# Performance work log

Hardware: AMD Instinct MI355X
Metric: run time of the kernel (lower is better)

Reference implementation:

```python
import jax, jax.numpy as jnp
import numpy as np

ALPHA = 0.2
N_NODES = 50000
N_REL = 500
E = 500000
E_NHOP = 100000


def l2norm(v):
    n = jnp.sqrt(jnp.sum(v * v, axis=1, keepdims=True))
    return v / jnp.maximum(n, 1e-12)


def sp_attention(x, src, dst, edge_embed, a, a2, concat):
    # a: [out, 2*din + drel]; edge_m = a @ cat(x[src], x[dst], edge_embed).T, done blockwise
    N, din = x.shape
    a_src, a_dst, a_rel = a[:, :din], a[:, din:2 * din], a[:, 2 * din:]
    edge_m = x[src] @ a_src.T + x[dst] @ a_dst.T + edge_embed @ a_rel.T  # [E, out]
    powers = -jax.nn.leaky_relu(edge_m @ a2, ALPHA)                      # [E]
    edge_e = jnp.exp(powers)
    e_rowsum = jax.ops.segment_sum(edge_e, src, num_segments=N)
    e_rowsum = jnp.where(e_rowsum == 0.0, 1e-12, e_rowsum)
    h_prime = jax.ops.segment_sum(edge_e[:, None] * edge_m, src, num_segments=N)
    h_prime = h_prime / e_rowsum[:, None]
    return jax.nn.elu(h_prime) if concat else h_prime


def spgat(x, rel, src, dst, edge_type, et_nhop, head_params, W, out_a, out_a2):
    ee = jnp.concatenate([rel[edge_type], rel[et_nhop[:, 0]] + rel[et_nhop[:, 1]]], axis=0)
    x = jnp.concatenate([sp_attention(x, src, dst, ee, a, a2, True) for a, a2 in head_params], axis=1)
    out_rel = rel @ W
    ee2 = jnp.concatenate([out_rel[edge_type], out_rel[et_nhop[:, 0]] + out_rel[et_nhop[:, 1]]], axis=0)
    x = jax.nn.elu(sp_attention(x, src, dst, ee2, out_a, out_a2, False))
    return x, out_rel


def forward_impl(entity_emb, relation_emb, W_entities,
                 g0_a0, g0_s0, g0_a1, g0_s1, g0_W, g0_oa, g0_os,
                 g1_a0, g1_s0, g1_W, g1_oa, g1_os,
                 edge_list, edge_type, train_indices_nhop, batch_inputs):
    ent = l2norm(entity_emb)
    rel = l2norm(relation_emb)
    # n-hop edges: (col3 -> col0), relation pair in cols 1,2
    src = jnp.concatenate([edge_list[0], train_indices_nhop[:, 3]])
    dst = jnp.concatenate([edge_list[1], train_indices_nhop[:, 0]])
    et_nhop = train_indices_nhop[:, 1:3]
    mask = jnp.zeros((ent.shape[0],), ent.dtype).at[batch_inputs[:, 2]].set(1.0)
    # layer 0 (2 heads)
    ent_up = ent @ W_entities
    rel_up = rel @ W_entities
    e_new, r_new = spgat(ent, rel, src, dst, edge_type, et_nhop,
                         [(g0_a0, g0_s0), (g0_a1, g0_s1)], g0_W, g0_oa, g0_os)
    ent = l2norm(ent_up + mask[:, None] * e_new)
    rel = l2norm(rel_up + r_new)
    # layer 1 (1 head, residual)
    e_new, r_new = spgat(ent, rel, src, dst, edge_type, et_nhop,
                         [(g1_a0, g1_s0)], g1_W, g1_oa, g1_os)
    ent = l2norm(ent + mask[:, None] * e_new)
    rel = l2norm(rel + r_new)
    return ent, rel


def setup_inputs() -> dict:
    key = jax.random.key(0)
    ks = jax.random.split(key, 20)
    s = 0.05
    inp = {
        "entity_emb": jax.random.normal(ks[0], (N_NODES, 100), jnp.float32),
        "relation_emb": jax.random.normal(ks[1], (N_REL, 100), jnp.float32),
        "W_entities": jax.random.normal(ks[2], (100, 200), jnp.float32) * s,
        "g0_a0": jax.random.normal(ks[3], (100, 300), jnp.float32) * s,
        "g0_s0": jax.random.normal(ks[4], (100,), jnp.float32) * s,
        "g0_a1": jax.random.normal(ks[5], (100, 300), jnp.float32) * s,
        "g0_s1": jax.random.normal(ks[6], (100,), jnp.float32) * s,
        "g0_W": jax.random.normal(ks[7], (100, 200), jnp.float32) * s,
        "g0_oa": jax.random.normal(ks[8], (200, 600), jnp.float32) * s,
        "g0_os": jax.random.normal(ks[9], (200,), jnp.float32) * s,
        "g1_a0": jax.random.normal(ks[10], (200, 600), jnp.float32) * s,
        "g1_s0": jax.random.normal(ks[11], (200,), jnp.float32) * s,
        "g1_W": jax.random.normal(ks[12], (200, 200), jnp.float32) * s,
        "g1_oa": jax.random.normal(ks[13], (200, 600), jnp.float32) * s,
        "g1_os": jax.random.normal(ks[14], (200,), jnp.float32) * s,
        "edge_list": jax.random.randint(ks[15], (2, E), 0, N_NODES, jnp.int64 if jax.config.jax_enable_x64 else jnp.int32),
        "edge_type": jax.random.randint(ks[16], (E,), 0, N_REL),
        "train_indices_nhop": jax.random.randint(ks[17], (E_NHOP, 4), 0, N_REL),
        "batch_inputs": jax.random.randint(ks[18], (10000, 3), 0, N_NODES),
    }
    return inp


def reference(entity_emb, relation_emb, W_entities,
              g0_a0, g0_s0, g0_a1, g0_s1, g0_W, g0_oa, g0_os,
              g1_a0, g1_s0, g1_W, g1_oa, g1_os,
              edge_list, edge_type, train_indices_nhop, batch_inputs):
    return forward_impl(entity_emb, relation_emb, W_entities,
                        g0_a0, g0_s0, g0_a1, g0_s1, g0_W, g0_oa, g0_os,
                        g1_a0, g1_s0, g1_W, g1_oa, g1_os,
                        edge_list, edge_type, train_indices_nhop, batch_inputs)
```

## Files before the change

### kernel.cpp

```cpp
#include <hip/hip_runtime.h>
#include <hip/hip_bf16.h>
#include <cstdint>
#include <cstddef>

#define NNODES 50000
#define NRELS  500
#define NEDGE  500000
#define NETOT  600000
#define MP     50048
#define RPAD   512
#define HOTN   512

typedef __attribute__((ext_vector_type(8))) short bf16x8;
typedef __attribute__((ext_vector_type(4))) float f32x4;

__device__ inline float bf2f(unsigned short s){
  union { unsigned u; float f; } v; v.u = ((unsigned)s) << 16; return v.f;
}
__device__ inline unsigned short f2bf(float f){
  __hip_bfloat16 h = __float2bfloat16(f);
  return __builtin_bit_cast(unsigned short, h);
}
__device__ inline float rl_f(float v, int i){
  return __builtin_bit_cast(float, __builtin_amdgcn_readlane(__builtin_bit_cast(int, v), i));
}

struct WEnt { int src, ld, boff, rows, K, tr, dstoff, Kp, rp; };
__device__ const WEnt g_went[18] = {
  {0,200,0,200,100,1,      0,128,256},
  {3,200,0,200,100,1,  32768,128,256},
  {1,300,  0,100,100,0,  65536,128,128},
  {1,300,100,100,100,0,  81920,128,128},
  {2,300,  0,100,100,0,  98304,128,128},
  {2,300,100,100,100,0, 114688,128,128},
  {1,300,200,100,100,0, 131072,128,128},
  {2,300,200,100,100,0, 147456,128,128},
  {4,600,  0,200,200,0, 163840,224,256},
  {4,600,200,200,200,0, 221184,224,256},
  {4,600,400,200,200,0, 278528,224,256},
  {5,600,  0,200,200,0, 335872,224,256},
  {5,600,200,200,200,0, 393216,224,256},
  {5,600,400,200,200,0, 450560,224,256},
  {6,200,0,200,200,1,   507904,224,256},
  {7,600,  0,200,200,0, 565248,224,256},
  {7,600,200,200,200,0, 622592,224,256},
  {7,600,400,200,200,0, 679936,224,256},
};
struct Ptr8 { const float* p[8]; };

#define SB_O1 587
#define SB_O2 599
#define SB_O3 620
#define SB_O4 641
#define SB_O5 650
#define SB_O6 5342
#define SB_O7 5351
#define SB_O8 13415
#define SB_O9 25915
#define SB_TOT 26040

struct SetupArgs {
  int* iall;
  __hip_bfloat16 *aent0, *ax1, *aent1, *arel0, *arel1;
  float* wt;
  const float *s0h, *s1h, *os0, *s1l, *os1;
  __hip_bfloat16* wa;
  Ptr8 wsrcs;
  const float *entity, *relation;
};

__global__ __launch_bounds__(256) void k_setup(SetupArgs a){
  int bid = blockIdx.x, tid = threadIdx.x;
  if (bid < SB_O1){ int i = bid*256 + tid; if (i < 150001) a.iall[i] = 0; return; }
  if (bid < SB_O2){ int i = (bid-SB_O1)*256 + tid;
    ((int*)(a.aent0 + (size_t)NNODES*128))[i] = 0; return; }
  if (bid < SB_O3){ int i = (bid-SB_O2)*256 + tid;
    if (i < 5376) ((int*)(a.ax1 + (size_t)NNODES*224))[i] = 0; return; }
  if (bid < SB_O4){ int i = (bid-SB_O3)*256 + tid;
    if (i < 5376) ((int*)(a.aent1 + (size_t)NNODES*224))[i] = 0; return; }
  if (bid < SB_O5){ int i = (bid-SB_O4)*256 + tid;
    if (i < 768) ((int*)(a.arel0 + (size_t)NRELS*128))[i] = 0;
    else if (i < 2112) ((int*)(a.arel1 + (size_t)NRELS*224))[i - 768] = 0;
    return; }
  if (bid < SB_O6){ int i = (bid-SB_O5)*256 + tid;
    int r = i / 24, k = 200 + (i - r*24);
    a.ax1[(size_t)r*224 + k] = __float2bfloat16(0.f); return; }
  if (bid < SB_O7){
    int i = (bid-SB_O6)*256 + tid; if (i >= 2304) return;
    float v = 0.f;
    if (i < 512){ int c = i & 127; const float* s = (i < 256) ? a.s0h : a.s1h; if (c < 100) v = s[c]; }
    else if (i < 768){ int j2 = i - 512, c = j2 & 127; const float* s = (j2 < 128) ? a.s0h : a.s1h; if (c < 100) v = s[c]; }
    else { int j2 = i - 768, t = j2 >> 9, c = j2 & 255;
           const float* s = (t==0)?a.os0:(t==1)?a.s1l:a.os1; if (c < 200) v = s[c]; }
    a.wt[i] = v; return; }
  if (bid < SB_O8){
    int sb = bid - SB_O7;
    WEnt e = g_went[sb / 448];
    int i = (sb - (sb/448)*448)*256 + tid;
    if (i >= e.rp*e.Kp) return;
    int r = i / e.Kp, k = i - r*e.Kp;
    float v = 0.f;
    if (r < e.rows && k < e.K)
      v = e.tr ? a.wsrcs.p[e.src][(size_t)k*e.ld + r] : a.wsrcs.p[e.src][(size_t)r*e.ld + e.boff + k];
    a.wa[e.dstoff + i] = __float2bfloat16(v); return; }
  {
    int wave = tid >> 6, lane = tid & 63;
    const float* src; __hip_bfloat16* dst; int row;
// ... 75 lines not shown
  bool isE = n < NNODES;
  int row = isE ? n : n - NNODES;
  const __hip_bfloat16* b = (isE ? baseE : baseR) + (size_t)row*224;
  const __hip_bfloat16* h = (isE ? hE : hR) + (size_t)row*224;
  float m = isE ? mask[row] : 1.0f;
  int c = lane*4;
  float4 v = make_float4(0.f,0.f,0.f,0.f);
  if (c < 200){
    ushort4 bb = *(const ushort4*)(b + c);
    ushort4 hh = *(const ushort4*)(h + c);
    v.x = bf2f(bb.x) + m*bf2f(hh.x);
    v.y = bf2f(bb.y) + m*bf2f(hh.y);
    v.z = bf2f(bb.z) + m*bf2f(hh.z);
    v.w = bf2f(bb.w) + m*bf2f(hh.w);
  }
  float ss = v.x*v.x + v.y*v.y + v.z*v.z + v.w*v.w;
  #pragma unroll
  for (int o = 32; o; o >>= 1) ss += __shfl_xor(ss, o, 64);
  float sc = 1.0f / fmaxf(sqrtf(ss), 1e-12f);
  if constexpr (FINAL){
    if (c < 200){
      float* o = (isE ? outfE : outfR) + (size_t)row*200 + c;
      *(float4*)o = make_float4(v.x*sc, v.y*sc, v.z*sc, v.w*sc);
    }
  } else {
    if (c < 224){
      __hip_bfloat16* o = (isE ? outbE : outbR) + (size_t)row*224 + c;
      ushort4 w4; w4.x = f2bf(v.x*sc); w4.y = f2bf(v.y*sc); w4.z = f2bf(v.z*sc); w4.w = f2bf(v.w*sc);
      *(ushort4*)o = w4;
    }
  }
}

__global__ __launch_bounds__(256) void k_rowdot3(
    const __hip_bfloat16* __restrict__ XN, const float* __restrict__ wtN, int GN,
    float* __restrict__ n0, float* __restrict__ n1, float* __restrict__ n2, float* __restrict__ n3,
    const __hip_bfloat16* __restrict__ XR, const float* __restrict__ wtR, int GR,
    float* __restrict__ r0, float* __restrict__ r1)
{
  int wave = threadIdx.x >> 6, lane = threadIdx.x & 63;
  int b = blockIdx.x;
  if (b < 12500){
    int row = b*4 + wave;
    const __hip_bfloat16* xr = XN + (size_t)row*512 + lane*8;
    const float* wr = wtN + lane*8;
    float p = 0.f;
    #pragma unroll
    for (int k = 0; k < 2; k++){
      ushort4 x = *(const ushort4*)(xr + 4*k);
      float4 a = *(const float4*)(wr + 4*k);
      p += bf2f(x.x)*a.x + bf2f(x.y)*a.y + bf2f(x.z)*a.z + bf2f(x.w)*a.w;
    }
    for (int o = GN>>1; o; o >>= 1) p += __shfl_xor(p, o, 64);
    if ((lane & (GN-1)) == 0){
      int g = lane / GN;
      float* out = (g==0)?n0:(g==1)?n1:(g==2)?n2:n3;
      out[row] = p;
    }
  } else {
    int row = (b - 12500)*4 + wave;
    if (row >= NRELS + 1) return;
    const __hip_bfloat16* xr = XR + (size_t)row*256 + lane*4;
    ushort4 x = *(const ushort4*)xr;
    float4 a = *(const float4*)(wtR + lane*4);
    float p = bf2f(x.x)*a.x + bf2f(x.y)*a.y + bf2f(x.z)*a.z + bf2f(x.w)*a.w;
    for (int o = GR>>1; o; o >>= 1) p += __shfl_xor(p, o, 64);
    if ((lane & (GR-1)) == 0){
      int g = lane / GR;
      float* out = (g==0)?r0:r1;
      out[row] = p;
    }
  }
}

struct GemmDesc {
  const __hip_bfloat16 *A, *B; __hip_bfloat16* C;
  int M, Nn, Kp, ldc, gx, nblk;
};
__global__ __launch_bounds__(256) void k_gemm2(GemmDesc g1, GemmDesc g2)
{
  __shared__ __hip_bfloat16 As[128*32];
  __shared__ __hip_bfloat16 Bs[64*32];
  const int tid = threadIdx.x;
  const int wave = tid >> 6, lane = tid & 63;
  const int lg = lane >> 4, li = lane & 15;
  int nwg = gridDim.x;
  int orig = blockIdx.x;
  int q = nwg >> 3, r = nwg & 7;
  int xcd = orig & 7, off = orig >> 3;
  int wg = (xcd < r ? xcd*(q+1) : r*(q+1) + (xcd - r)*q) + off;
  GemmDesc g = (wg < g1.nblk) ? g1 : g2;
  int local = (wg < g1.nblk) ? wg : wg - g1.nblk;
  const int bx = local % g.gx, by = local / g.gx;
  const int m0 = by * 128, n0 = bx * 64;
  const int Kp = g.Kp;
  const int wr = wave >> 1, wc = wave & 1;
  f32x4 acc[4][2] = {};

  const int ar0 = tid >> 2;
  const int ar1 = (tid + 256) >> 2;
  const int ap  = tid & 3;
  const char* Ab = (const char*)g.A;
  const char* Bb = (const char*)g.B;
  char* asB = (char*)As;
  char* bsB = (char*)Bs;

  for (int kk = 0; kk < Kp; kk += 32){
    {
      int p0 = ap ^ ((ar0 >> 1) & 3);
      const char* s0 = Ab + ((size_t)(m0 + ar0)*Kp + kk)*2 + p0*16;
// ... 13 lines not shown
    #pragma unroll
    for (int mf = 0; mf < 4; mf++){
      int row = wr*64 + mf*16 + li;
      int p = lg ^ ((row >> 1) & 3);
      av[mf] = *(const bf16x8*)(asB + row*64 + p*16);
    }
    #pragma unroll
    for (int nf = 0; nf < 2; nf++){
      int row = wc*32 + nf*16 + li;
      int p = lg ^ ((row >> 1) & 3);
      bv[nf] = *(const bf16x8*)(bsB + row*64 + p*16);
    }
    #pragma unroll
    for (int mf = 0; mf < 4; mf++)
      #pragma unroll
      for (int nf = 0; nf < 2; nf++)
        acc[mf][nf] = __builtin_amdgcn_mfma_f32_16x16x32_bf16(av[mf], bv[nf], acc[mf][nf], 0, 0, 0);
    __syncthreads();
  }
  #pragma unroll
  for (int mf = 0; mf < 4; mf++){
    #pragma unroll
    for (int nf = 0; nf < 2; nf++){
      int gc = n0 + wc*32 + nf*16 + li;
      if (gc >= g.Nn) continue;
      int gr0 = m0 + wr*64 + mf*16 + lg*4;
      #pragma unroll
      for (int rr = 0; rr < 4; rr++){
        int gr = gr0 + rr;
        if (gr < g.M) g.C[(size_t)gr*g.ldc + gc] = __float2bfloat16(acc[mf][nf][rr]);
      }
    }
  }
}

__device__ inline void agg6_edges(int bstart, int end, int bstep,
    const int4* __restrict__ erec, float psn,
    const float* __restrict__ pd, const float* __restrict__ prs,
    const __hip_bfloat16* __restrict__ xdb, int ldx,
    const __hip_bfloat16* __restrict__ rrb, int ldr,
    int lane, float& Sl, float4& acc)
{
  const bool act = lane < 50;
  const int co = 4*lane;
  for (int b = bstart; b < end; b += bstep){
    int j = b + lane;
    int4 e = make_int4(0, NRELS, NRELS, 0);
    float wv = 0.f;
    if (j < end){
      e = erec[j];
      float lg = psn + pd[e.x] + prs[e.y] + prs[e.z];
      wv = __expf(-((lg > 0.f) ? lg : 0.2f*lg));
    }
    Sl += wv;
    int m = end - b; if (m > 64) m = 64;
    if (act){
      #pragma unroll 8
      for (int i = 0; i < m; ++i){
        float w0 = rl_f(wv, i);
        int d  = __builtin_amdgcn_readlane(e.x, i);
        int t0 = __builtin_amdgcn_readlane(e.y, i);
        int t1 = __builtin_amdgcn_readlane(e.z, i);
        const __hip_bfloat16* xr  = xdb + (size_t)d*ldx;
        const __hip_bfloat16* rr0 = rrb + (size_t)t0*ldr;
        ushort4 xa = *(const ushort4*)(xr + co);
        ushort4 ra = *(const ushort4*)(rr0 + co);
        float sx = bf2f(xa.x)+bf2f(ra.x), sy = bf2f(xa.y)+bf2f(ra.y);
        float sz = bf2f(xa.z)+bf2f(ra.z), sw = bf2f(xa.w)+bf2f(ra.w);
        if (t1 != NRELS){
          const __hip_bfloat16* rr1 = rrb + (size_t)t1*ldr;
          ushort4 rc = *(const ushort4*)(rr1 + co);
          sx += bf2f(rc.x); sy += bf2f(rc.y); sz += bf2f(rc.z); sw += bf2f(rc.w);
        }
        acc.x += w0*sx; acc.y += w0*sy; acc.z += w0*sz; acc.w += w0*sw;
      }
    }
  }
}

__device__ inline void agg5_finalize(int n, float S, float4 acc, int lane,
    const __hip_bfloat16* __restrict__ XSD, int cxs,
    __hip_bfloat16* __restrict__ outb, int ldb, int coffb)
{
  if (lane >= 50) return;
  float inv = (S > 0.f) ? 1.0f/S : 0.f;
  ushort4 xs4 = *(const ushort4*)(XSD + (size_t)n*512 + cxs + 4*lane);
  float h0 = (S > 0.f) ? bf2f(xs4.x) + acc.x*inv : 0.f;
  float h1 = (S > 0.f) ? bf2f(xs4.y) + acc.y*inv : 0.f;
  float h2 = (S > 0.f) ? bf2f(xs4.z) + acc.z*inv : 0.f;
  float h3 = (S > 0.f) ? bf2f(xs4.w) + acc.w*inv : 0.f;
  h0 = (h0 > 0.f) ? h0 : expm1f(h0);
  h1 = (h1 > 0.f) ? h1 : expm1f(h1);
  h2 = (h2 > 0.f) ? h2 : expm1f(h2);
  h3 = (h3 > 0.f) ? h3 : expm1f(h3);
  ushort4 o; o.x = f2bf(h0); o.y = f2bf(h1); o.z = f2bf(h2); o.w = f2bf(h3);
  *(ushort4*)(outb + (size_t)n*ldb + coffb + 4*lane) = o;
}

__global__ __launch_bounds__(256) void k_agg5(
    const int* __restrict__ rowofs, const int4* __restrict__ erec,
    const float* __restrict__ ps, const float* __restrict__ pd, const float* __restrict__ prs,
    const __hip_bfloat16* __restrict__ XSD,
    const __hip_bfloat16* __restrict__ RRb,
    __hip_bfloat16* __restrict__ outb, int ldb, int coffb)
{
  __shared__ float4 redA[256];
  __shared__ float redS[4];
  int bid = blockIdx.x;
  int wave = threadIdx.x >> 6, lane = threadIdx.x & 63;
  const __hip_bfloat16* xdb = XSD + 256;

  if (bid < HOTN){
    int n = bid;
    int beg = rowofs[n], end = rowofs[n+1];
    float psn = ps[n];
    float Sl = 0.f;
    float4 acc = make_float4(0.f,0.f,0.f,0.f);
    agg6_edges(beg + wave*64, end, 256, erec, psn, pd, prs,
               xdb, 512, RRb, 256, lane, Sl, acc);
    float Sw = Sl;
    #pragma unroll
    for (int o = 32; o; o >>= 1) Sw += __shfl_xor(Sw, o, 64);
    redA[threadIdx.x] = acc;
    if (lane == 0) redS[wave] = Sw;
    __syncthreads();
    if (wave == 0){
      float4 a0 = redA[lane], a1 = redA[lane+64], a2 = redA[lane+128], a3 = redA[lane+192];
      float4 at = make_float4(a0.x+a1.x+a2.x+a3.x, a0.y+a1.y+a2.y+a3.y,
                              a0.z+a1.z+a2.z+a3.z, a0.w+a1.w+a2.w+a3.w);
      float St = redS[0] + redS[1] + redS[2] + redS[3];
      agg5_finalize(n, St, at, lane, XSD, 0, outb, ldb, coffb);
    }
  } else {
    int n = HOTN + (bid - HOTN)*4 + wave;
    int beg = rowofs[n], end = rowofs[n+1];
    float psn = ps[n];
    float Sl = 0.f;
    float4 acc = make_float4(0.f,0.f,0.f,0.f);
    agg6_edges(beg, end, 64, erec, psn, pd, prs,
               xdb, 512, RRb, 256, lane, Sl, acc);
    float S = Sl;
    #pragma unroll
    for (int o = 32; o; o >>= 1) S += __shfl_xor(S, o, 64);
    agg5_finalize(n, S, acc, lane, XSD, 0, outb, ldb, coffb);
  }
}

__device__ inline void agg6h_edges(int bstart, int end, int bstep,
    const int4* __restrict__ erec,
    float ps0n, const float* __restrict__ pd0, const float* __restrict__ prs0,
    float ps1n, const float* __restrict__ pd1, const float* __restrict__ prs1,
    const __hip_bfloat16* __restrict__ XSD, const __hip_bfloat16* __restrict__ RRb,
    int lane, float& Sl0, float& Sl1, float4& acc)
{
  const bool act = lane < 50;
  const int head = (lane >= 25) ? 1 : 0;
  const int li = lane - 25*head;
  const int loffX = (head ? 384 : 128) + 4*li;
  const int loffR = (head ? 128 : 0) + 4*li;
  for (int b = bstart; b < end; b += bstep){
    int j = b + lane;
    int4 e = make_int4(0, NRELS, NRELS, 0);
    float wv0 = 0.f, wv1 = 0.f;
    if (j < end){
      e = erec[j];
      float lg0 = ps0n + pd0[e.x] + prs0[e.y] + prs0[e.z];
      float lg1 = ps1n + pd1[e.x] + prs1[e.y] + prs1[e.z];
      wv0 = __expf(-((lg0 > 0.f) ? lg0 : 0.2f*lg0));
      wv1 = __expf(-((lg1 > 0.f) ? lg1 : 0.2f*lg1));
    }
    Sl0 += wv0; Sl1 += wv1;
    int m = end - b; if (m > 64) m = 64;
    if (act){
      #pragma unroll 8
      for (int i = 0; i < m; ++i){
        float wH0 = rl_f(wv0, i);
        float wH1 = rl_f(wv1, i);
        int d  = __builtin_amdgcn_readlane(e.x, i);
        int t0 = __builtin_amdgcn_readlane(e.y, i);
        int t1 = __builtin_amdgcn_readlane(e.z, i);
        float w = head ? wH1 : wH0;
        const __hip_bfloat16* xr = XSD + (size_t)d*512;
        const __hip_bfloat16* r0 = RRb + (size_t)t0*256;
        ushort4 xa = *(const ushort4*)(xr + loffX);
        ushort4 ra = *(const ushort4*)(r0 + loffR);
        float sx = bf2f(xa.x)+bf2f(ra.x), sy = bf2f(xa.y)+bf2f(ra.y);
        float sz = bf2f(xa.z)+bf2f(ra.z), sw = bf2f(xa.w)+bf2f(ra.w);
        if (t1 != NRELS){
          const __hip_bfloat16* r1 = RRb + (size_t)t1*256;
          ushort4 rc = *(const ushort4*)(r1 + loffR);
          sx += bf2f(rc.x); sy += bf2f(rc.y); sz += bf2f(rc.z); sw += bf2f(rc.w);
        }
        acc.x += w*sx; acc.y += w*sy; acc.z += w*sz; acc.w += w*sw;
      }
    }
  }
}

__device__ inline void aggh_finalize(int n, float S0, float S1, float4 acc, int lane,
    const __hip_bfloat16* __restrict__ XSD,
    __hip_bfloat16* __restrict__ outb, int ldb)
{
  if (lane >= 50) return;
  int head = (lane >= 25) ? 1 : 0;
  int li = lane - 25*head;
  float S = head ? S1 : S0;
  float inv = (S > 0.f) ? 1.0f/S : 0.f;
  ushort4 xs4 = *(const ushort4*)(XSD + (size_t)n*512 + (head ? 256 : 0) + 4*li);
  float h0 = (S > 0.f) ? bf2f(xs4.x) + acc.x*inv : 0.f;
  float h1 = (S > 0.f) ? bf2f(xs4.y) + acc.y*inv : 0.f;
  float h2 = (S > 0.f) ? bf2f(xs4.z) + acc.z*inv : 0.f;
  float h3 = (S > 0.f) ? bf2f(xs4.w) + acc.w*inv : 0.f;
  h0 = (h0 > 0.f) ? h0 : expm1f(h0);
  h1 = (h1 > 0.f) ? h1 : expm1f(h1);
  h2 = (h2 > 0.f) ? h2 : expm1f(h2);
  h3 = (h3 > 0.f) ? h3 : expm1f(h3);
  ushort4 o; o.x = f2bf(h0); o.y = f2bf(h1); o.z = f2bf(h2); o.w = f2bf(h3);
  *(ushort4*)(outb + (size_t)n*ldb + 100*head + 4*li) = o;
}

__global__ __launch_bounds__(256) void k_aggh(
    const int* __restrict__ rowofs, const int4* __restrict__ erec,
    const float* __restrict__ ps0, const float* __restrict__ pd0, const float* __restrict__ prs0,
    const float* __restrict__ ps1, const float* __restrict__ pd1, const float* __restrict__ prs1,
    const __hip_bfloat16* __restrict__ XSD, const __hip_bfloat16* __restrict__ RRb,
    __hip_bfloat16* __restrict__ outb, int ldb)
{
  __shared__ float4 redA[256];
  __shared__ float redS0[4];
  __shared__ float redS1[4];
  int bid = blockIdx.x;
  int wave = threadIdx.x >> 6, lane = threadIdx.x & 63;

  if (bid < HOTN){
    int n = bid;
    int beg = rowofs[n], end = rowofs[n+1];
    float ps0n = ps0[n], ps1n = ps1[n];
    float Sl0 = 0.f, Sl1 = 0.f;
    float4 acc = make_float4(0.f,0.f,0.f,0.f);
    agg6h_edges(beg + wave*64, end, 256, erec, ps0n, pd0, prs0, ps1n, pd1, prs1,
                XSD, RRb, lane, Sl0, Sl1, acc);
    float Sw0 = Sl0, Sw1 = Sl1;
    #pragma unroll
    for (int o = 32; o; o >>= 1){ Sw0 += __shfl_xor(Sw0, o, 64); Sw1 += __shfl_xor(Sw1, o, 64); }
    redA[threadIdx.x] = acc;
    if (lane == 0){ redS0[wave] = Sw0; redS1[wave] = Sw1; }
    __syncthreads();
    if (wave == 0){
      float4 a0 = redA[lane], a1 = redA[lane+64], a2 = redA[lane+128], a3 = redA[lane+192];
      float4 at = make_float4(a0.x+a1.x+a2.x+a3.x, a0.y+a1.y+a2.y+a3.y,
                              a0.z+a1.z+a2.z+a3.z, a0.w+a1.w+a2.w+a3.w);
      float St0 = redS0[0] + redS0[1] + redS0[2] + redS0[3];
      float St1 = redS1[0] + redS1[1] + redS1[2] + redS1[3];
      aggh_finalize(n, St0, St1, at, lane, XSD, outb, ldb);
    }
  } else {
    int n = HOTN + (bid - HOTN)*4 + wave;
    int beg = rowofs[n], end = rowofs[n+1];
    float ps0n = ps0[n], ps1n = ps1[n];
    float Sl0 = 0.f, Sl1 = 0.f;
    float4 acc = make_float4(0.f,0.f,0.f,0.f);
    agg6h_edges(beg, end, 64, erec, ps0n, pd0, prs0, ps1n, pd1, prs1,
                XSD, RRb, lane, Sl0, Sl1, acc);
    float S0 = Sl0, S1 = Sl1;
    #pragma unroll
    for (int o = 32; o; o >>= 1){ S0 += __shfl_xor(S0, o, 64); S1 += __shfl_xor(S1, o, 64); }
    aggh_finalize(n, S0, S1, acc, lane, XSD, outb, ldb);
  }
}

extern "C" void kernel_launch(void* const* d_in, const int* in_sizes, int n_in,
                              void* d_out, int out_size, void* d_ws, size_t ws_size,
                              hipStream_t stream) {
  const float* entity   = (const float*)d_in[0];
  const float* relation = (const float*)d_in[1];
  const float* W_ent    = (const float*)d_in[2];
  const float* g0_a0    = (const float*)d_in[3];
  const float* g0_s0    = (const float*)d_in[4];
  const float* g0_a1    = (const float*)d_in[5];
  const float* g0_s1    = (const float*)d_in[6];
  const float* g0_W     = (const float*)d_in[7];
  const float* g0_oa    = (const float*)d_in[8];
  const float* g0_os    = (const float*)d_in[9];
  const float* g1_a0    = (const float*)d_in[10];
  const float* g1_s0    = (const float*)d_in[11];
  const float* g1_W     = (const float*)d_in[12];
  const float* g1_oa    = (const float*)d_in[13];
  const float* g1_os    = (const float*)d_in[14];
  const int*   el       = (const int*)d_in[15];
  const int*   et       = (const int*)d_in[16];
  const int*   nh       = (const int*)d_in[17];
  const int*   batch    = (const int*)d_in[18];
  (void)in_sizes; (void)n_in; (void)out_size; (void)ws_size;

  char* w = (char*)d_ws;
  auto alloc = [&](size_t bytes)->char*{ char* p = w; w += (bytes + 255) & ~(size_t)255; return p; };
  float* PS0   = (float*)alloc((size_t)NNODES*4);
  float* PD0   = (float*)alloc((size_t)NNODES*4);
  float* PS1   = (float*)alloc((size_t)NNODES*4);
  float* PD1   = (float*)alloc((size_t)NNODES*4);
  float* PRS0  = (float*)alloc((size_t)(NRELS+4)*4);
  float* PRS1  = (float*)alloc((size_t)(NRELS+4)*4);
  float* WT    = (float*)alloc((size_t)2304*4);
  __hip_bfloat16* AENT0  = (__hip_bfloat16*)alloc((size_t)MP*128*2);
  __hip_bfloat16* AX1    = (__hip_bfloat16*)alloc((size_t)MP*224*2);
  __hip_bfloat16* AENT1  = (__hip_bfloat16*)alloc((size_t)MP*224*2);
  __hip_bfloat16* ENTUPb = (__hip_bfloat16*)alloc((size_t)MP*224*2);
  __hip_bfloat16* HB     = (__hip_bfloat16*)alloc((size_t)MP*224*2);
  __hip_bfloat16* AREL0  = (__hip_bfloat16*)alloc((size_t)RPAD*128*2);
  __hip_bfloat16* AREL1  = (__hip_bfloat16*)alloc((size_t)RPAD*224*2);
  __hip_bfloat16* RELUPb = (__hip_bfloat16*)alloc((size_t)RPAD*224*2);
  __hip_bfloat16* ORb0   = (__hip_bfloat16*)alloc((size_t)RPAD*224*2);
  __hip_bfloat16* ORb1   = (__hip_bfloat16*)alloc((size_t)RPAD*224*2);
  __hip_bfloat16* XSD    = (__hip_bfloat16*)alloc((size_t)MP*512*2);
  __hip_bfloat16* RRb    = (__hip_bfloat16*)alloc((size_t)RPAD*256*2);
  __hip_bfloat16* WA     = (__hip_bfloat16*)alloc((size_t)737280*2);
  int* IALL = (int*)alloc((size_t)150001*4);
  int* ROWOFS = IALL;
  int* CUR    = IALL + 50001;
  float* MASK = (float*)(IALL + 100001);
  int4* EREC  = (int4*)alloc((size_t)NETOT*16);
  int* PART   = (int*)alloc((size_t)256*4);

  const __hip_bfloat16* WET   = WA;
  const __hip_bfloat16* G0WT  = WA + 32768;
  const __hip_bfloat16* BH0   = WA + 65536;
  const __hip_bfloat16* BR0   = WA + 131072;
  const __hip_bfloat16* BO0   = WA + 163840;
  const __hip_bfloat16* BO0r  = WA + 278528;
  const __hip_bfloat16* BA1   = WA + 335872;
  const __hip_bfloat16* BA1r  = WA + 450560;
  const __hip_bfloat16* G1WT  = WA + 507904;
  const __hip_bfloat16* BO1   = WA + 565248;
  const __hip_bfloat16* BO1r  = WA + 679936;

  float* outEnt = (float*)d_out;
  float* outRel = outEnt + (size_t)NNODES*200;

  const int TB = 256;
  auto gb = [&](long long n){ return (int)((n + TB - 1)/TB); };
  const int AGG_GRID = HOTN + (NNODES - HOTN)/4;
  const int RD_GRID = 12500 + 126;

  {
    SetupArgs a;
    a.iall = IALL; a.aent0 = AENT0; a.ax1 = AX1; a.aent1 = AENT1; a.arel0 = AREL0; a.arel1 = AREL1;
    a.wt = WT; a.s0h = g0_s0; a.s1h = g0_s1; a.os0 = g0_os; a.s1l = g1_s0; a.os1 = g1_os;
    a.wa = WA;
    a.wsrcs.p[0] = W_ent; a.wsrcs.p[1] = g0_a0; a.wsrcs.p[2] = g0_a1; a.wsrcs.p[3] = g0_W;
    a.wsrcs.p[4] = g0_oa; a.wsrcs.p[5] = g1_a0; a.wsrcs.p[6] = g1_W;  a.wsrcs.p[7] = g1_oa;
    a.entity = entity; a.relation = relation;
    k_setup<<<SB_TOT, 256, 0, stream>>>(a);
  }
  k_mask_set<<<gb(10000), TB, 0, stream>>>(batch, MASK, 10000);
  k_hist<<<gb(NETOT), TB, 0, stream>>>(el, nh, ROWOFS);
  int nsb = (NNODES + 255)/256;
  k_scan1<<<nsb, 256, 0, stream>>>(ROWOFS, NNODES, PART);
  k_scan2<<<1, 256, 0, stream>>>(PART, nsb);
  k_scan3<<<nsb, 256, 0, stream>>>(ROWOFS, NNODES, PART);
  k_scatter<<<gb(NETOT), TB, 0, stream>>>(el, et, nh, ROWOFS, CUR, EREC);

  auto mkdesc = [](const __hip_bfloat16* A, const __hip_bfloat16* B, __hip_bfloat16* C,
                   int M, int Nn, int Kp, int ldc){
    GemmDesc d; d.A = A; d.B = B; d.C = C; d.M = M; d.Nn = Nn; d.Kp = Kp; d.ldc = ldc;
    d.gx = (Nn + 63)/64; d.nblk = d.gx * ((M + 127)/128); return d;
  };
  GemmDesc dnull = {}; dnull.nblk = 0;
  auto gemm2 = [&](GemmDesc d1, GemmDesc d2){
    k_gemm2<<<d1.nblk + d2.nblk, 256, 0, stream>>>(d1, d2);
  };

  gemm2(mkdesc(AENT0, WET, ENTUPb, MP, 200, 128, 224),
        mkdesc(AREL0, WET, RELUPb, RPAD, 200, 128, 224));

  gemm2(mkdesc(AENT0, BH0, XSD, MP, 512, 128, 512),
        mkdesc(AREL0, BR0, RRb, RPAD, 256, 128, 256));
  k_rowdot3<<<RD_GRID, 256, 0, stream>>>(XSD, WT + 0, 16, PS0, PD0, PS1, PD1,
                                         RRb, WT + 512, 32, PRS0, PRS1);
  k_aggh<<<AGG_GRID, 256, 0, stream>>>(ROWOFS, EREC, PS0, PD0, PRS0, PS1, PD1, PRS1,
                                       XSD, RRb, AX1, 224);

  gemm2(mkdesc(AX1, BO0, XSD, MP, 512, 224, 512),
        mkdesc(AREL0, G0WT, ORb0, RPAD, 224, 128, 224));
  gemm2(mkdesc(ORb0, BO0r, RRb, RPAD, 256, 224, 256), dnull);
  k_rowdot3<<<RD_GRID, 256, 0, stream>>>(XSD, WT + 768, 32, PS0, PD0, nullptr, nullptr,
                                         RRb, WT + 768, 64, PRS0, nullptr);
  k_agg5<<<AGG_GRID, 256, 0, stream>>>(ROWOFS, EREC, PS0, PD0, PRS0, XSD, RRb, HB, 224, 0);
  k_combine2<false><<<NNODES + NRELS, 64, 0, stream>>>(ENTUPb, HB, MASK, RELUPb, ORb0,
      nullptr, nullptr, AENT1, AREL1);

  gemm2(mkdesc(AENT1, BA1, XSD, MP, 512, 224, 512),
        mkdesc(AREL1, BA1r, RRb, RPAD, 256, 224, 256));
  k_rowdot3<<<RD_GRID, 256, 0, stream>>>(XSD, WT + 1280, 32, PS0, PD0, nullptr, nullptr,
                                         RRb, WT + 1280, 64, PRS0, nullptr);
  k_agg5<<<AGG_GRID, 256, 0, stream>>>(ROWOFS, EREC, PS0, PD0, PRS0, XSD, RRb, AX1, 224, 0);

  gemm2(mkdesc(AX1, BO1, XSD, MP, 512, 224, 512),
        mkdesc(AREL1, G1WT, ORb1, RPAD, 224, 224, 224));
  gemm2(mkdesc(ORb1, BO1r, RRb, RPAD, 256, 224, 256), dnull);
  k_rowdot3<<<RD_GRID, 256, 0, stream>>>(XSD, WT + 1792, 32, PS0, PD0, nullptr, nullptr,
                                         RRb, WT + 1792, 64, PRS0, nullptr);
  k_agg5<<<AGG_GRID, 256, 0, stream>>>(ROWOFS, EREC, PS0, PD0, PRS0, XSD, RRb, HB, 224, 0);

  k_combine2<true><<<NNODES + NRELS, 64, 0, stream>>>(AENT1, HB, MASK, AREL1, ORb1,
      outEnt, outRel, nullptr, nullptr);
}
```

Baseline: 612.2 us.

## Fuse attention row-dot products into GEMM epilogue via atomics; rework edge gather loop

Removes the separate k_rowdot3 kernels by computing the per-row dot products with the attention vector inside the GEMM epilogue. Each wave reduces its partial sums across lanes and atomically adds them into zero-initialised per-layer score buffers, which the setup kernel now clears. The aggregation edge loops also change: they broadcast edge data with __shfl instead of readlane and process two edges per iteration with separate accumulators to expose more memory parallelism. In exchange the change adds float atomics, which make the sums order-dependent, plus extra buffers to zero.

```diff
diff --git a/kernel.cpp b/kernel.cpp
--- a/kernel.cpp
+++ b/kernel.cpp
@@ -20,9 +20,6 @@
 __device__ inline unsigned short f2bf(float f){
   __hip_bfloat16 h = __float2bfloat16(f);
   return __builtin_bit_cast(unsigned short, h);
-}
-__device__ inline float rl_f(float v, int i){
-  return __builtin_bit_cast(float, __builtin_amdgcn_readlane(__builtin_bit_cast(int, v), i));
 }
 
 struct WEnt { int src, ld, boff, rows, K, tr, dstoff, Kp, rp; };
@@ -49,18 +46,21 @@
 struct Ptr8 { const float* p[8]; };
 
 #define SB_O1 587
-#define SB_O2 599
-#define SB_O3 620
-#define SB_O4 641
-#define SB_O5 650
-#define SB_O6 5342
-#define SB_O7 5351
-#define SB_O8 13415
-#define SB_O9 25915
-#define SB_TOT 26040
+#define SB_OZ 2552
+#define SB_O2 2564
+#define SB_O3 2585
+#define SB_O4 2606
+#define SB_O5 2615
+#define SB_O6 7307
+#define SB_O7 7316
+#define SB_O8 15380
+#define SB_O9 27880
+#define SB_TOT 28005
+#define NPSALL 503040
 
 struct SetupArgs {
   int* iall;
+  float* psall;
   __hip_bfloat16 *aent0, *ax1, *aent1, *arel0, *arel1;
   float* wt;
   const float *s0h, *s1h, *os0, *s1l, *os1;
@@ -72,7 +72,9 @@
 __global__ __launch_bounds__(256) void k_setup(SetupArgs a){
   int bid = blockIdx.x, tid = threadIdx.x;
   if (bid < SB_O1){ int i = bid*256 + tid; if (i < 150001) a.iall[i] = 0; return; }
-  if (bid < SB_O2){ int i = (bid-SB_O1)*256 + tid;
+  if (bid < SB_OZ){ int i = (bid-SB_O1)*256 + tid;
+    if (i < NPSALL) a.psall[i] = 0.f; return; }
+  if (bid < SB_O2){ int i = (bid-SB_OZ)*256 + tid;
     ((int*)(a.aent0 + (size_t)NNODES*128))[i] = 0; return; }
   if (bid < SB_O3){ int i = (bid-SB_O2)*256 + tid;
     if (i < 5376) ((int*)(a.ax1 + (size_t)NNODES*224))[i] = 0; return; }
@@ -214,50 +216,11 @@
   }
 }
 
-__global__ __launch_bounds__(256) void k_rowdot3(
-    const __hip_bfloat16* __restrict__ XN, const float* __restrict__ wtN, int GN,
-    float* __restrict__ n0, float* __restrict__ n1, float* __restrict__ n2, float* __restrict__ n3,
-    const __hip_bfloat16* __restrict__ XR, const float* __restrict__ wtR, int GR,
-    float* __restrict__ r0, float* __restrict__ r1)
-{
-  int wave = threadIdx.x >> 6, lane = threadIdx.x & 63;
-  int b = blockIdx.x;
-  if (b < 12500){
-    int row = b*4 + wave;
-    const __hip_bfloat16* xr = XN + (size_t)row*512 + lane*8;
-    const float* wr = wtN + lane*8;
-    float p = 0.f;
-    #pragma unroll
-    for (int k = 0; k < 2; k++){
-      ushort4 x = *(const ushort4*)(xr + 4*k);
-      float4 a = *(const float4*)(wr + 4*k);
-      p += bf2f(x.x)*a.x + bf2f(x.y)*a.y + bf2f(x.z)*a.z + bf2f(x.w)*a.w;
-    }
-    for (int o = GN>>1; o; o >>= 1) p += __shfl_xor(p, o, 64);
-    if ((lane & (GN-1)) == 0){
-      int g = lane / GN;
-      float* out = (g==0)?n0:(g==1)?n1:(g==2)?n2:n3;
-      out[row] = p;
-    }
-  } else {
-    int row = (b - 12500)*4 + wave;
-    if (row >= NRELS + 1) return;
-    const __hip_bfloat16* xr = XR + (size_t)row*256 + lane*4;
-    ushort4 x = *(const ushort4*)xr;
-    float4 a = *(const float4*)(wtR + lane*4);
-    float p = bf2f(x.x)*a.x + bf2f(x.y)*a.y + bf2f(x.z)*a.z + bf2f(x.w)*a.w;
-    for (int o = GR>>1; o; o >>= 1) p += __shfl_xor(p, o, 64);
-    if ((lane & (GR-1)) == 0){
-      int g = lane / GR;
-      float* out = (g==0)?r0:r1;
-      out[row] = p;
-    }
-  }
-}
-
 struct GemmDesc {
   const __hip_bfloat16 *A, *B; __hip_bfloat16* C;
-  int M, Nn, Kp, ldc, gx, nblk;
+  int M, Nn, Kp, ldc, gx, nblk, dotM;
+  const float* wt;
+  float* dout[4];
 };
 __global__ __launch_bounds__(256) void k_gemm2(GemmDesc g1, GemmDesc g2)
 {
@@ -337,17 +300,36 @@
       }
     }
   }
-}
-
-__device__ inline void agg6_edges(int bstart, int end, int bstep,
+  if (g.wt){
+    float* dp = g.dout[n0 >> 7];
+    float w0 = g.wt[n0 + wc*32 + li];
+    float w1 = g.wt[n0 + wc*32 + 16 + li];
+    #pragma unroll
+    for (int mf = 0; mf < 4; mf++){
+      #pragma unroll
+      for (int rr = 0; rr < 4; rr++){
+        float p = acc[mf][0][rr]*w0 + acc[mf][1][rr]*w1;
+        p += __shfl_xor(p, 1, 64); p += __shfl_xor(p, 2, 64);
+        p += __shfl_xor(p, 4, 64); p += __shfl_xor(p, 8, 64);
+        int gr = m0 + wr*64 + mf*16 + lg*4 + rr;
+        if (li == 0 && gr < g.dotM) atomicAdd(dp + gr, p);
+      }
+    }
+  }
+}
+
+__device__ inline void agg5_edges(int bstart, int end, int bstep,
     const int4* __restrict__ erec, float psn,
     const float* __restrict__ pd, const float* __restrict__ prs,
-    const __hip_bfloat16* __restrict__ xdb, int ldx,
-    const __hip_bfloat16* __restrict__ rrb, int ldr,
-    int lane, float& Sl, float4& acc)
+    const __hip_bfloat16* __restrict__ XSD, int ldx, int cxd,
+    const __hip_bfloat16* __restrict__ RRb, int ldr, int crr,
+    int lane, float& Sl, float4& accO)
 {
-  const bool act = lane < 50;
-  const int co = 4*lane;
+  bool act = lane < 50;
+  const __hip_bfloat16* xb = XSD + cxd + 4*lane;
+  const __hip_bfloat16* rb = RRb + crr + 4*lane;
+  float4 accA = make_float4(0.f,0.f,0.f,0.f);
+  float4 accB = make_float4(0.f,0.f,0.f,0.f);
   for (int b = bstart; b < end; b += bstep){
     int j = b + lane;
     int4 e = make_int4(0, NRELS, NRELS, 0);
@@ -359,37 +341,59 @@
     }
     Sl += wv;
     int m = end - b; if (m > 64) m = 64;
-    if (act){
-      #pragma unroll 8
-      for (int i = 0; i < m; ++i){
-        float w0 = rl_f(wv, i);
-        int d  = __builtin_amdgcn_readlane(e.x, i);
-        int t0 = __builtin_amdgcn_readlane(e.y, i);
-        int t1 = __builtin_amdgcn_readlane(e.z, i);
-        const __hip_bfloat16* xr  = xdb + (size_t)d*ldx;
-        const __hip_bfloat16* rr0 = rrb + (size_t)t0*ldr;
-        ushort4 xa = *(const ushort4*)(xr + co);
-        ushort4 ra = *(const ushort4*)(rr0 + co);
-        float sx = bf2f(xa.x)+bf2f(ra.x), sy = bf2f(xa.y)+bf2f(ra.y);
-        float sz = bf2f(xa.z)+bf2f(ra.z), sw = bf2f(xa.w)+bf2f(ra.w);
-        if (t1 != NRELS){
-          const __hip_bfloat16* rr1 = rrb + (size_t)t1*ldr;
-          ushort4 rc = *(const ushort4*)(rr1 + co);
-          sx += bf2f(rc.x); sy += bf2f(rc.y); sz += bf2f(rc.z); sw += bf2f(rc.w);
+    int i = 0;
+    for (; i + 1 < m; i += 2){
+      float wA = __shfl(wv, i),   wB = __shfl(wv, i+1);
+      int dA = __shfl(e.x, i),   tA0 = __shfl(e.y, i),   tA1 = __shfl(e.z, i);
+      int dB = __shfl(e.x, i+1), tB0 = __shfl(e.y, i+1), tB1 = __shfl(e.z, i+1);
+      if (act){
+        ushort4 xA = *(const ushort4*)(xb + (size_t)dA*ldx);
+        ushort4 rA = *(const ushort4*)(rb + (size_t)tA0*ldr);
+        ushort4 xB = *(const ushort4*)(xb + (size_t)dB*ldx);
+        ushort4 rB = *(const ushort4*)(rb + (size_t)tB0*ldr);
+        float ax = bf2f(xA.x)+bf2f(rA.x), ay = bf2f(xA.y)+bf2f(rA.y);
+        float az = bf2f(xA.z)+bf2f(rA.z), aw = bf2f(xA.w)+bf2f(rA.w);
+        if (tA1 != NRELS){
+          ushort4 rc = *(const ushort4*)(rb + (size_t)tA1*ldr);
+          ax += bf2f(rc.x); ay += bf2f(rc.y); az += bf2f(rc.z); aw += bf2f(rc.w);
         }
-        acc.x += w0*sx; acc.y += w0*sy; acc.z += w0*sz; acc.w += w0*sw;
+        float bx = bf2f(xB.x)+bf2f(rB.x), by = bf2f(xB.y)+bf2f(rB.y);
+        float bz = bf2f(xB.z)+bf2f(rB.z), bw = bf2f(xB.w)+bf2f(rB.w);
+        if (tB1 != NRELS){
+          ushort4 rc = *(const ushort4*)(rb + (size_t)tB1*ldr);
+          bx += bf2f(rc.x); by += bf2f(rc.y); bz += bf2f(rc.z); bw += bf2f(rc.w);
+        }
+        accA.x += wA*ax; accA.y += wA*ay; accA.z += wA*az; accA.w += wA*aw;
+        accB.x += wB*bx; accB.y += wB*by; accB.z += wB*bz; accB.w += wB*bw;
       }
     }
-  }
+    if (i < m){
+      float wA = __shfl(wv, i);
+      int dA = __shfl(e.x, i), tA0 = __shfl(e.y, i), tA1 = __shfl(e.z, i);
+      if (act){
+        ushort4 xA = *(const ushort4*)(xb + (size_t)dA*ldx);
+        ushort4 rA = *(const ushort4*)(rb + (size_t)tA0*ldr);
+        float ax = bf2f(xA.x)+bf2f(rA.x), ay = bf2f(xA.y)+bf2f(rA.y);
+        float az = bf2f(xA.z)+bf2f(rA.z), aw = bf2f(xA.w)+bf2f(rA.w);
+        if (tA1 != NRELS){
+          ushort4 rc = *(const ushort4*)(rb + (size_t)tA1*ldr);
+          ax += bf2f(rc.x); ay += bf2f(rc.y); az += bf2f(rc.z); aw += bf2f(rc.w);
+        }
+        accA.x += wA*ax; accA.y += wA*ay; accA.z += wA*az; accA.w += wA*aw;
+      }
+    }
+  }
+  accO.x += accA.x + accB.x; accO.y += accA.y + accB.y;
+  accO.z += accA.z + accB.z; accO.w += accA.w + accB.w;
 }
 
 __device__ inline void agg5_finalize(int n, float S, float4 acc, int lane,
-    const __hip_bfloat16* __restrict__ XSD, int cxs,
+    const __hip_bfloat16* __restrict__ XSD, int ldx, int cxs,
     __hip_bfloat16* __restrict__ outb, int ldb, int coffb)
 {
   if (lane >= 50) return;
   float inv = (S > 0.f) ? 1.0f/S : 0.f;
-  ushort4 xs4 = *(const ushort4*)(XSD + (size_t)n*512 + cxs + 4*lane);
+  ushort4 xs4 = *(const ushort4*)(XSD + (size_t)n*ldx + cxs + 4*lane);
   float h0 = (S > 0.f) ? bf2f(xs4.x) + acc.x*inv : 0.f;
   float h1 = (S > 0.f) ? bf2f(xs4.y) + acc.y*inv : 0.f;
   float h2 = (S > 0.f) ? bf2f(xs4.z) + acc.z*inv : 0.f;
@@ -413,7 +417,6 @@
   __shared__ float redS[4];
   int bid = blockIdx.x;
   int wave = threadIdx.x >> 6, lane = threadIdx.x & 63;
-  const __hip_bfloat16* xdb = XSD + 256;
 
   if (bid < HOTN){
     int n = bid;
@@ -421,8 +424,8 @@
     float psn = ps[n];
     float Sl = 0.f;
     float4 acc = make_float4(0.f,0.f,0.f,0.f);
-    agg6_edges(beg + wave*64, end, 256, erec, psn, pd, prs,
-               xdb, 512, RRb, 256, lane, Sl, acc);
+    agg5_edges(beg + wave*64, end, 256, erec, psn, pd, prs,
+               XSD, 512, 256, RRb, 256, 0, lane, Sl, acc);
     float Sw = Sl;
     #pragma unroll
     for (int o = 32; o; o >>= 1) Sw += __shfl_xor(Sw, o, 64);
@@ -434,7 +437,7 @@
       float4 at = make_float4(a0.x+a1.x+a2.x+a3.x, a0.y+a1.y+a2.y+a3.y,
                               a0.z+a1.z+a2.z+a3.z, a0.w+a1.w+a2.w+a3.w);
       float St = redS[0] + redS[1] + redS[2] + redS[3];
-      agg5_finalize(n, St, at, lane, XSD, 0, outb, ldb, coffb);
+      agg5_finalize(n, St, at, lane, XSD, 512, 0, outb, ldb, coffb);
     }
   } else {
     int n = HOTN + (bid - HOTN)*4 + wave;
@@ -442,27 +445,30 @@
     float psn = ps[n];
     float Sl = 0.f;
     float4 acc = make_float4(0.f,0.f,0.f,0.f);
-    agg6_edges(beg, end, 64, erec, psn, pd, prs,
-               xdb, 512, RRb, 256, lane, Sl, acc);
+    agg5_edges(beg, end, 64, erec, psn, pd, prs,
+               XSD, 512, 256, RRb, 256, 0, lane, Sl, acc);
     float S = Sl;
     #pragma unroll
     for (int o = 32; o; o >>= 1) S += __shfl_xor(S, o, 64);
-    agg5_finalize(n, S, acc, lane, XSD, 0, outb, ldb, coffb);
-  }
-}
-
-__device__ inline void agg6h_edges(int bstart, int end, int bstep,
+    agg5_finalize(n, S, acc, lane, XSD, 512, 0, outb, ldb, coffb);
+  }
+}
+
+__device__ inline void aggh_edges(int bstart, int end, int bstep,
     const int4* __restrict__ erec,
     float ps0n, const float* __restrict__ pd0, const float* __restrict__ prs0,
     float ps1n, const float* __restrict__ pd1, const float* __restrict__ prs1,
-    const __hip_bfloat16* __restrict__ XSD, const __hip_bfloat16* __restrict__ RRb,
-    int lane, float& Sl0, float& Sl1, float4& acc)
+    const __hip_bfloat16* __restrict__ XSD, int ldx,
+    const __hip_bfloat16* __restrict__ RRb, int ldr,
+    int lane, float& Sl0, float& Sl1, float4& accO)
 {
-  const bool act = lane < 50;
-  const int head = (lane >= 25) ? 1 : 0;
-  const int li = lane - 25*head;
-  const int loffX = (head ? 384 : 128) + 4*li;
-  const int loffR = (head ? 128 : 0) + 4*li;
+  bool act = lane < 50;
+  int head = (lane >= 25) ? 1 : 0;
+  int li = lane - 25*head;
+  const __hip_bfloat16* xb = XSD + (head ? 384 : 128) + 4*li;
+  const __hip_bfloat16* rb = RRb + (head ? 128 : 0) + 4*li;
+  float4 accA = make_float4(0.f,0.f,0.f,0.f);
+  float4 accB = make_float4(0.f,0.f,0.f,0.f);
   for (int b = bstart; b < end; b += bstep){
     int j = b + lane;
     int4 e = make_int4(0, NRELS, NRELS, 0);
@@ -476,30 +482,54 @@
     }
     Sl0 += wv0; Sl1 += wv1;
     int m = end - b; if (m > 64) m = 64;
-    if (act){
-      #pragma unroll 8
-      for (int i = 0; i < m; ++i){
-        float wH0 = rl_f(wv0, i);
-        float wH1 = rl_f(wv1, i);
-        int d  = __builtin_amdgcn_readlane(e.x, i);
-        int t0 = __builtin_amdgcn_readlane(e.y, i);
-        int t1 = __builtin_amdgcn_readlane(e.z, i);
-        float w = head ? wH1 : wH0;
-        const __hip_bfloat16* xr = XSD + (size_t)d*512;
-        const __hip_bfloat16* r0 = RRb + (size_t)t0*256;
-        ushort4 xa = *(const ushort4*)(xr + loffX);
-        ushort4 ra = *(const ushort4*)(r0 + loffR);
-        float sx = bf2f(xa.x)+bf2f(ra.x), sy = bf2f(xa.y)+bf2f(ra.y);
-        float sz = bf2f(xa.z)+bf2f(ra.z), sw = bf2f(xa.w)+bf2f(ra.w);
-        if (t1 != NRELS){
-          const __hip_bfloat16* r1 = RRb + (size_t)t1*256;
-          ushort4 rc = *(const ushort4*)(r1 + loffR);
-          sx += bf2f(rc.x); sy += bf2f(rc.y); sz += bf2f(rc.z); sw += bf2f(rc.w);
+    int i = 0;
+    for (; i + 1 < m; i += 2){
+      float wA0 = __shfl(wv0, i),   wA1 = __shfl(wv1, i);
+      float wB0 = __shfl(wv0, i+1), wB1 = __shfl(wv1, i+1);
+      int dA = __shfl(e.x, i),   tA0 = __shfl(e.y, i),   tA1 = __shfl(e.z, i);
+      int dB = __shfl(e.x, i+1), tB0 = __shfl(e.y, i+1), tB1 = __shfl(e.z, i+1);
+      if (act){
+        float wA = head ? wA1 : wA0;
+        float wB = head ? wB1 : wB0;
+        ushort4 xA = *(const ushort4*)(xb + (size_t)dA*ldx);
+        ushort4 rA = *(const ushort4*)(rb + (size_t)tA0*ldr);
+        ushort4 xB = *(const ushort4*)(xb + (size_t)dB*ldx);
+        ushort4 rB = *(const ushort4*)(rb + (size_t)tB0*ldr);
+        float ax = bf2f(xA.x)+bf2f(rA.x), ay = bf2f(xA.y)+bf2f(rA.y);
+        float az = bf2f(xA.z)+bf2f(rA.z), aw = bf2f(xA.w)+bf2f(rA.w);
+        if (tA1 != NRELS){
+          ushort4 rc = *(const ushort4*)(rb + (size_t)tA1*ldr);
+          ax += bf2f(rc.x); ay += bf2f(rc.y); az += bf2f(rc.z); aw += bf2f(rc.w);
         }
-        acc.x += w*sx; acc.y += w*sy; acc.z += w*sz; acc.w += w*sw;
+        float bx = bf2f(xB.x)+bf2f(rB.x), by = bf2f(xB.y)+bf2f(rB.y);
+        float bz = bf2f(xB.z)+bf2f(rB.z), bw = bf2f(xB.w)+bf2f(rB.w);
+        if (tB1 != NRELS){
+          ushort4 rc = *(const ushort4*)(rb + (size_t)tB1*ldr);
+          bx += bf2f(rc.x); by += bf2f(rc.y); bz += bf2f(rc.z); bw += bf2f(rc.w);
+        }
+        accA.x += wA*ax; accA.y += wA*ay; accA.z += wA*az; accA.w += wA*aw;
+        accB.x += wB*bx; accB.y += wB*by; accB.z += wB*bz; accB.w += wB*bw;
       }
     }
-  }
+    if (i < m){
+      float wA0 = __shfl(wv0, i), wA1 = __shfl(wv1, i);
+      int dA = __shfl(e.x, i), tA0 = __shfl(e.y, i), tA1 = __shfl(e.z, i);
+      if (act){
+        float wA = head ? wA1 : wA0;
+        ushort4 xA = *(const ushort4*)(xb + (size_t)dA*ldx);
+        ushort4 rA = *(const ushort4*)(rb + (size_t)tA0*ldr);
+        float ax = bf2f(xA.x)+bf2f(rA.x), ay = bf2f(xA.y)+bf2f(rA.y);
+        float az = bf2f(xA.z)+bf2f(rA.z), aw = bf2f(xA.w)+bf2f(rA.w);
+        if (tA1 != NRELS){
+          ushort4 rc = *(const ushort4*)(rb + (size_t)tA1*ldr);
+          ax += bf2f(rc.x); ay += bf2f(rc.y); az += bf2f(rc.z); aw += bf2f(rc.w);
+        }
+        accA.x += wA*ax; accA.y += wA*ay; accA.z += wA*az; accA.w += wA*aw;
+      }
+    }
+  }
+  accO.x += accA.x + accB.x; accO.y += accA.y + accB.y;
+  accO.z += accA.z + accB.z; accO.w += accA.w + accB.w;
 }
 
 __device__ inline void aggh_finalize(int n, float S0, float S1, float4 acc, int lane,
@@ -543,8 +573,8 @@
     float ps0n = ps0[n], ps1n = ps1[n];
     float Sl0 = 0.f, Sl1 = 0.f;
     float4 acc = make_float4(0.f,0.f,0.f,0.f);
-    agg6h_edges(beg + wave*64, end, 256, erec, ps0n, pd0, prs0, ps1n, pd1, prs1,
-                XSD, RRb, lane, Sl0, Sl1, acc);
+    aggh_edges(beg + wave*64, end, 256, erec, ps0n, pd0, prs0, ps1n, pd1, prs1,
+               XSD, 512, RRb, 256, lane, Sl0, Sl1, acc);
     float Sw0 = Sl0, Sw1 = Sl1;
     #pragma unroll
     for (int o = 32; o; o >>= 1){ Sw0 += __shfl_xor(Sw0, o, 64); Sw1 += __shfl_xor(Sw1, o, 64); }
@@ -565,8 +595,8 @@
     float ps0n = ps0[n], ps1n = ps1[n];
     float Sl0 = 0.f, Sl1 = 0.f;
     float4 acc = make_float4(0.f,0.f,0.f,0.f);
-    agg6h_edges(beg, end, 64, erec, ps0n, pd0, prs0, ps1n, pd1, prs1,
-                XSD, RRb, lane, Sl0, Sl1, acc);
+    aggh_edges(beg, end, 64, erec, ps0n, pd0, prs0, ps1n, pd1, prs1,
+               XSD, 512, RRb, 256, lane, Sl0, Sl1, acc);
     float S0 = Sl0, S1 = Sl1;
     #pragma unroll
     for (int o = 32; o; o >>= 1){ S0 += __shfl_xor(S0, o, 64); S1 += __shfl_xor(S1, o, 64); }
@@ -600,12 +630,14 @@
 
   char* w = (char*)d_ws;
   auto alloc = [&](size_t bytes)->char*{ char* p = w; w += (bytes + 255) & ~(size_t)255; return p; };
-  float* PS0   = (float*)alloc((size_t)NNODES*4);
-  float* PD0   = (float*)alloc((size_t)NNODES*4);
-  float* PS1   = (float*)alloc((size_t)NNODES*4);
-  float* PD1   = (float*)alloc((size_t)NNODES*4);
-  float* PRS0  = (float*)alloc((size_t)(NRELS+4)*4);
-  float* PRS1  = (float*)alloc((size_t)(NRELS+4)*4);
+  float* PSALL = (float*)alloc((size_t)NPSALL*4);
+  float* PS0 = PSALL,          * PD0 = PSALL + 50048;
+  float* PS1 = PSALL + 100096, * PD1 = PSALL + 150144;
+  float* PS2 = PSALL + 200192, * PD2 = PSALL + 250240;
+  float* PS3 = PSALL + 300288, * PD3 = PSALL + 350336;
+  float* PS4 = PSALL + 400384, * PD4 = PSALL + 450432;
+  float* PRS0 = PSALL + 500480, * PRS1 = PSALL + 500992;
+  float* PRS2 = PSALL + 501504, * PRS3 = PSALL + 502016, * PRS4 = PSALL + 502528;
   float* WT    = (float*)alloc((size_t)2304*4);
   __hip_bfloat16* AENT0  = (__hip_bfloat16*)alloc((size_t)MP*128*2);
   __hip_bfloat16* AX1    = (__hip_bfloat16*)alloc((size_t)MP*224*2);
@@ -645,11 +677,11 @@
   const int TB = 256;
   auto gb = [&](long long n){ return (int)((n + TB - 1)/TB); };
   const int AGG_GRID = HOTN + (NNODES - HOTN)/4;
-  const int RD_GRID = 12500 + 126;
 
   {
     SetupArgs a;
-    a.iall = IALL; a.aent0 = AENT0; a.ax1 = AX1; a.aent1 = AENT1; a.arel0 = AREL0; a.arel1 = AREL1;
+    a.iall = IALL; a.psall = PSALL;
+    a.aent0 = AENT0; a.ax1 = AX1; a.aent1 = AENT1; a.arel0 = AREL0; a.arel1 = AREL1;
     a.wt = WT; a.s0h = g0_s0; a.s1h = g0_s1; a.os0 = g0_os; a.s1l = g1_s0; a.os1 = g1_os;
     a.wa = WA;
     a.wsrcs.p[0] = W_ent; a.wsrcs.p[1] = g0_a0; a.wsrcs.p[2] = g0_a1; a.wsrcs.p[3] = g0_W;
@@ -666,46 +698,41 @@
   k_scatter<<<gb(NETOT), TB, 0, stream>>>(el, et, nh, ROWOFS, CUR, EREC);
 
   auto mkdesc = [](const __hip_bfloat16* A, const __hip_bfloat16* B, __hip_bfloat16* C,
-                   int M, int Nn, int Kp, int ldc){
+                   int M, int Nn, int Kp, int ldc,
+                   const float* wt, float* q0, float* q1, float* q2, float* q3, int dotM){
     GemmDesc d; d.A = A; d.B = B; d.C = C; d.M = M; d.Nn = Nn; d.Kp = Kp; d.ldc = ldc;
-    d.gx = (Nn + 63)/64; d.nblk = d.gx * ((M + 127)/128); return d;
+    d.gx = (Nn + 63)/64; d.nblk = d.gx * ((M + 127)/128);
+    d.wt = wt; d.dout[0] = q0; d.dout[1] = q1; d.dout[2] = q2; d.dout[3] = q3; d.dotM = dotM;
+    return d;
   };
   GemmDesc dnull = {}; dnull.nblk = 0;
   auto gemm2 = [&](GemmDesc d1, GemmDesc d2){
     k_gemm2<<<d1.nblk + d2.nblk, 256, 0, stream>>>(d1, d2);
   };
 
-  gemm2(mkdesc(AENT0, WET, ENTUPb, MP, 200, 128, 224),
-        mkdesc(AREL0, WET, RELUPb, RPAD, 200, 128, 224));
-
-  gemm2(mkdesc(AENT0, BH0, XSD, MP, 512, 128, 512),
-        mkdesc(AREL0, BR0, RRb, RPAD, 256, 128, 256));
-  k_rowdot3<<<RD_GRID, 256, 0, stream>>>(XSD, WT + 0, 16, PS0, PD0, PS1, PD1,
-                                         RRb, WT + 512, 32, PRS0, PRS1);
+  gemm2(mkdesc(AENT0, WET, ENTUPb, MP, 200, 128, 224, nullptr,0,0,0,0,0),
+        mkdesc(AREL0, WET, RELUPb, RPAD, 200, 128, 224, nullptr,0,0,0,0,0));
+
+  gemm2(mkdesc(AENT0, BH0, XSD, MP, 512, 128, 512, WT + 0, PS0, PD0, PS1, PD1, NNODES),
+        mkdesc(AREL0, BR0, RRb, RPAD, 256, 128, 256, WT + 512, PRS0, PRS1, 0, 0, RPAD));
   k_aggh<<<AGG_GRID, 256, 0, stream>>>(ROWOFS, EREC, PS0, PD0, PRS0, PS1, PD1, PRS1,
                                        XSD, RRb, AX1, 224);
 
-  gemm2(mkdesc(AX1, BO0, XSD, MP, 512, 224, 512),
-        mkdesc(AREL0, G0WT, ORb0, RPAD, 224, 128, 224));
-  gemm2(mkdesc(ORb0, BO0r, RRb, RPAD, 256, 224, 256), dnull);
-  k_rowdot3<<<RD_GRID, 256, 0, stream>>>(XSD, WT + 768, 32, PS0, PD0, nullptr, nullptr,
-                                         RRb, WT + 768, 64, PRS0, nullptr);
-  k_agg5<<<AGG_GRID, 256, 0, stream>>>(ROWOFS, EREC, PS0, PD0, PRS0, XSD, RRb, HB, 224, 0);
+  gemm2(mkdesc(AX1, BO0, XSD, MP, 512, 224, 512, WT + 768, PS2, PS2, PD2, PD2, NNODES),
+        mkdesc(AREL0, G0WT, ORb0, RPAD, 224, 128, 224, nullptr,0,0,0,0,0));
+  gemm2(mkdesc(ORb0, BO0r, RRb, RPAD, 256, 224, 256, WT + 768, PRS2, PRS2, 0, 0, RPAD), dnull);
+  k_agg5<<<AGG_GRID, 256, 0, stream>>>(ROWOFS, EREC, PS2, PD2, PRS2, XSD, RRb, HB, 224, 0);
   k_combine2<false><<<NNODES + NRELS, 64, 0, stream>>>(ENTUPb, HB, MASK, RELUPb, ORb0,
       nullptr, nullptr, AENT1, AREL1);
 
-  gemm2(mkdesc(AENT1, BA1, XSD, MP, 512, 224, 512),
-        mkdesc(AREL1, BA1r, RRb, RPAD, 256, 224, 256));
-  k_rowdot3<<<RD_GRID, 256, 0, stream>>>(XSD, WT + 1280, 32, PS0, PD0, nullptr, nullptr,
-                                         RRb, WT + 1280, 64, PRS0, nullptr);
-  k_agg5<<<AGG_GRID, 256, 0, stream>>>(ROWOFS, EREC, PS0, PD0, PRS0, XSD, RRb, AX1, 224, 0);
-
-  gemm2(mkdesc(AX1, BO1, XSD, MP, 512, 224, 512),
-        mkdesc(AREL1, G1WT, ORb1, RPAD, 224, 224, 224));
-  gemm2(mkdesc(ORb1, BO1r, RRb, RPAD, 256, 224, 256), dnull);
-  k_rowdot3<<<RD_GRID, 256, 0, stream>>>(XSD, WT + 1792, 32, PS0, PD0, nullptr, nullptr,
-                                         RRb, WT + 1792, 64, PRS0, nullptr);
-  k_agg5<<<AGG_GRID, 256, 0, stream>>>(ROWOFS, EREC, PS0, PD0, PRS0, XSD, RRb, HB, 224, 0);
+  gemm2(mkdesc(AENT1, BA1, XSD, MP, 512, 224, 512, WT + 1280, PS3, PS3, PD3, PD3, NNODES),
+        mkdesc(AREL1, BA1r, RRb, RPAD, 256, 224, 256, WT + 1280, PRS3, PRS3, 0, 0, RPAD));
+  k_agg5<<<AGG_GRID, 256, 0, stream>>>(ROWOFS, EREC, PS3, PD3, PRS3, XSD, RRb, AX1, 224, 0);
+
+  gemm2(mkdesc(AX1, BO1, XSD, MP, 512, 224, 512, WT + 1792, PS4, PS4, PD4, PD4, NNODES),
+        mkdesc(AREL1, G1WT, ORb1, RPAD, 224, 224, 224, nullptr,0,0,0,0,0));
+  gemm2(mkdesc(ORb1, BO1r, RRb, RPAD, 256, 224, 256, WT + 1792, PRS4, PRS4, 0, 0, RPAD), dnull);
+  k_agg5<<<AGG_GRID, 256, 0, stream>>>(ROWOFS, EREC, PS4, PD4, PRS4, XSD, RRb, HB, 224, 0);
 
   k_combine2<true><<<NNODES + NRELS, 64, 0, stream>>>(AENT1, HB, MASK, AREL1, ORb1,
       outEnt, outRel, nullptr, nullptr);
```

After: 657.9 us. +7.5%, slower.
